# Kernel tuning notes

Measured on AMD Instinct MI355X. Metric: run time of the kernel, lower is better.

## Reference

```python
import jax, jax.numpy as jnp
import numpy as np

R, K = 16, 64  # rel_size (heads), key_size (head dim)
LN_EPS = 1e-5


def apply_rope(x, pos):
    # pos: [B,S,1,K], halves are sin/cos; x: [B,S,R,K]
    sin, cos = jnp.split(pos, 2, axis=-1)
    x0, x1 = jnp.split(x, 2, axis=-1)
    return jnp.concatenate([x0 * cos - x1 * sin, x0 * sin + x1 * cos], axis=-1)


def setup_inputs() -> dict:
    key = jax.random.key(0)
    ks = jax.random.split(key, 6)
    B, S, H = 2, 2048, 1024
    x = jax.random.normal(ks[0], (B, S, H), dtype=jnp.float32)
    pos = jax.random.uniform(ks[1], (B, S, 1, K), dtype=jnp.float32)
    W_qkv = jax.random.normal(ks[2], (H, R * K * 3), dtype=jnp.float32) * (H ** -0.5)
    b_qkv = jax.random.normal(ks[3], (R * K * 3,), dtype=jnp.float32) * 0.02
    W_out = jax.random.normal(ks[4], (R * K, H), dtype=jnp.float32) * ((R * K) ** -0.5)
    b_out = jax.random.normal(ks[5], (H,), dtype=jnp.float32) * 0.02
    ln_g = jnp.ones((H,), dtype=jnp.float32)
    ln_b = jnp.zeros((H,), dtype=jnp.float32)
    return {"x": x, "pos": pos, "W_qkv": W_qkv, "b_qkv": b_qkv,
            "W_out": W_out, "b_out": b_out, "ln_g": ln_g, "ln_b": ln_b}


def reference(x, pos, W_qkv, b_qkv, W_out, b_out, ln_g, ln_b):
    B, S, H = x.shape
    qkv = (x @ W_qkv + b_qkv).reshape(B, S, R, 3 * K)
    q, k, v = jnp.split(qkv, 3, axis=-1)  # each [B,S,R,K]
    k = k / jnp.linalg.norm(k, axis=-1, keepdims=True)
    q = apply_rope(q, pos)
    k = apply_rope(k, pos)
    # SDPA with scale=1 (as in the original call)
    scores = jnp.einsum('bqhd,bkhd->bhqk', q, k)
    attn = jax.nn.softmax(scores, axis=-1)
    ctx = jnp.einsum('bhqk,bkhd->bqhd', attn, v).reshape(B, S, R * K)
    postx = ctx @ W_out + b_out
    y = x + postx
    mu = jnp.mean(y, axis=-1, keepdims=True)
    var = jnp.mean(jnp.square(y - mu), axis=-1, keepdims=True)
    return (y - mu) * jax.lax.rsqrt(var + LN_EPS) * ln_g + ln_b
```

## Files before the change

kernel.cpp:

```cpp
#include <hip/hip_runtime.h>


#define B_   2
#define S_   2048
#define H_   1024
#define R_   16
#define BS_  (B_*S_)
#define NQKV 3072
#define LOG2E 1.44269504088896f

typedef float    floatx4 __attribute__((ext_vector_type(4)));
typedef _Float16 half8   __attribute__((ext_vector_type(8)));
typedef _Float16 half4   __attribute__((ext_vector_type(4)));
typedef __fp16   fp16x2  __attribute__((ext_vector_type(2)));

#if __has_builtin(__builtin_amdgcn_exp2f)
#define EXP2(x) __builtin_amdgcn_exp2f(x)
#else
#define EXP2(x) exp2f(x)
#endif

__device__ __forceinline__ void gl_lds16(const _Float16* g, _Float16* l) {
    __builtin_amdgcn_global_load_lds(
        (const __attribute__((address_space(1))) unsigned int*)g,
        (__attribute__((address_space(3))) unsigned int*)l, 16, 0, 0);
}

__global__ __launch_bounds__(256) void cast_f16_kernel(
    const float* __restrict__ in, _Float16* __restrict__ out, int n)
{
    int i = (blockIdx.x * 256 + threadIdx.x) * 4;
    if (i >= n) return;
    float4 v = *(const float4*)(in + i);
    half4 h;
    h.x = (_Float16)v.x; h.y = (_Float16)v.y; h.z = (_Float16)v.z; h.w = (_Float16)v.w;
    *(half4*)(out + i) = h;
}

__global__ __launch_bounds__(256) void transpose_cast_f16(
    const float* __restrict__ in, _Float16* __restrict__ out, int rows, int cols)
{
    __shared__ float tile[32][33];
    int bx = blockIdx.x * 32;
    int by = blockIdx.y * 32;
    int tx = threadIdx.x & 31, ty = threadIdx.x >> 5;
#pragma unroll
    for (int i = 0; i < 32; i += 8)
        tile[ty + i][tx] = in[(size_t)(by + ty + i) * cols + bx + tx];
    __syncthreads();
#pragma unroll
    for (int i = 0; i < 32; i += 8)
        out[(size_t)(bx + ty + i) * rows + by + tx] = (_Float16)tile[tx][ty + i];
}

__global__ __launch_bounds__(256) void gemm_f16_mfma(
    const _Float16* __restrict__ A, const _Float16* __restrict__ Bt,
    const float* __restrict__ bias, const float* __restrict__ resid,
    float* __restrict__ C, int M, int N, int Kd)
{
    __shared__ _Float16 Als[128 * 32];
    __shared__ _Float16 Bls[128 * 32];
    int tid  = threadIdx.x;
    int lane = tid & 63, w = tid >> 6;
    int wr = w >> 1, wc = w & 1;
    int fr = lane & 15, fq = lane >> 4;
    int m0 = blockIdx.y * 128, n0 = blockIdx.x * 128;

    floatx4 acc[4][4] = {};

    const _Float16* ga[2]; const _Float16* gb[2];
    _Float16 *la[2], *lb[2];
#pragma unroll
    for (int i2 = 0; i2 < 2; ++i2) {
        int ch = 2 * w + i2;
        int row = ch * 16 + (lane >> 2), col = (lane & 3) * 8;
        ga[i2] = A  + (size_t)(m0 + row) * Kd + col;
        gb[i2] = Bt + (size_t)(n0 + row) * Kd + col;
        la[i2] = Als + ch * 512;
        lb[i2] = Bls + ch * 512;
    }

    for (int k0 = 0; k0 < Kd; k0 += 32) {
        __syncthreads();
#pragma unroll
        for (int i2 = 0; i2 < 2; ++i2) {
            gl_lds16(ga[i2] + k0, la[i2]);
            gl_lds16(gb[i2] + k0, lb[i2]);
        }
        __syncthreads();
        half8 af[4], bf[4];
#pragma unroll
        for (int i = 0; i < 4; ++i)
            af[i] = *(const half8*)(Als + (wr * 64 + i * 16 + fr) * 32 + fq * 8);
#pragma unroll
        for (int j = 0; j < 4; ++j)
            bf[j] = *(const half8*)(Bls + (wc * 64 + j * 16 + fr) * 32 + fq * 8);
#pragma unroll
        for (int i = 0; i < 4; ++i)
#pragma unroll
            for (int j = 0; j < 4; ++j)
                acc[i][j] = __builtin_amdgcn_mfma_f32_16x16x32_f16(
                    af[i], bf[j], acc[i][j], 0, 0, 0);
    }

#pragma unroll
    for (int i = 0; i < 4; ++i)
#pragma unroll
        for (int j = 0; j < 4; ++j)
#pragma unroll
            for (int r2 = 0; r2 < 4; ++r2) {
                int row = m0 + wr * 64 + i * 16 + fq * 4 + r2;
                int col = n0 + wc * 64 + j * 16 + fr;
                float v = acc[i][j][r2] + bias[col];
                if (resid) v += resid[(size_t)row * N + col];
                C[(size_t)row * N + col] = v;
            }
}

__global__ __launch_bounds__(256) void rope_kernel(
    const float* __restrict__ qkv, const float* __restrict__ pos,
    _Float16* __restrict__ qt, _Float16* __restrict__ kt)
{
    int task = blockIdx.x * 4 + (threadIdx.x >> 6);
    int lane = threadIdx.x & 63;
    int r = task & 15, bs = task >> 4;
    int b = bs >> 11, s = bs & 2047;

    const float* base = qkv + (size_t)bs * NQKV + r * 192;
    float qv = base[lane];
    float kv = base[64 + lane];

    float ss = kv * kv;
#pragma unroll
    for (int off = 32; off > 0; off >>= 1) ss += __shfl_xor(ss, off);
    kv *= rsqrtf(ss);

    int j = lane & 31;
    float sn = pos[(size_t)bs * 64 + j];
    float cs = pos[(size_t)bs * 64 + 32 + j];
    float qp = __shfl_xor(qv, 32);
    float kp = __shfl_xor(kv, 32);
    float qo, ko;
    if (lane < 32) { qo = qv * cs - qp * sn; ko = kv * cs - kp * sn; }
    else           { qo = qp * sn + qv * cs; ko = kp * sn + kv * cs; }

    size_t oidx = ((size_t)(b * 16 + r) * S_ + s) * 64 + lane;
    qt[oidx] = (_Float16)(qo * LOG2E);
    kt[oidx] = (_Float16)ko;
}

__global__ __launch_bounds__(256) void vtrans_kernel(
    const float* __restrict__ qkv, _Float16* __restrict__ vt2)
{
    __shared__ float tile[64][65];
    int head = blockIdx.x, tau = blockIdx.y;
    int s0 = tau * 64;
    int b = head >> 4, rh = head & 15;
    int tx = threadIdx.x & 63, ty = threadIdx.x >> 6;
#pragma unroll
    for (int si = ty; si < 64; si += 4)
        tile[si][tx] = qkv[(size_t)(b * S_ + s0 + si) * NQKV + rh * 192 + 128 + tx];
    __syncthreads();
    int P = tx;
    int op = P >> 3;
    int hi = (P >> 2) & 1, lo = P & 3;
#pragma unroll
    for (int d = ty; d < 64; d += 4) {
        int ol = op ^ (d & 7);
        int key = 32 * (ol >> 2) + 16 * hi + 4 * (ol & 3) + lo;
        vt2[(((size_t)head * 32 + tau) * 64 + d) * 64 + P] = (_Float16)tile[key][d];
    }
}

__global__ __launch_bounds__(256) void attn_mfma_kernel(
    const _Float16* __restrict__ qt, const _Float16* __restrict__ kt,
    const _Float16* __restrict__ vt2, _Float16* __restrict__ ctx)
{
    __shared__ _Float16 Kls[64 * 64];
    __shared__ _Float16 Vls[64 * 64];

    int head = blockIdx.x, q0 = blockIdx.y * 128;
    int b = head >> 4, rh = head & 15;
    int tid = threadIdx.x, lane = tid & 63, w = tid >> 6;
    int g = lane >> 4, c = lane & 15;

    half8 qf[2][2];
    float mL[2], l_s[2] = {0.f, 0.f};
#pragma unroll
    for (int qg = 0; qg < 2; ++qg) {
        const _Float16* qp =
            qt + ((size_t)head * S_ + q0 + w * 32 + qg * 16 + c) * 64 + 8 * g;
        qf[qg][0] = *(const half8*)qp;
        qf[qg][1] = *(const half8*)(qp + 32);
        float qq = 0.f;
#pragma unroll
        for (int i = 0; i < 8; ++i) {
            float a = (float)qf[qg][0][i], b2 = (float)qf[qg][1][i];
            qq += a * a + b2 * b2;
        }
        qq += __shfl_xor(qq, 16);
        qq += __shfl_xor(qq, 32);
        mL[qg] = sqrtf(qq);
    }

    floatx4 o_acc[2][4] = {};

    const _Float16* kg[2]; const _Float16* vg[2];
    _Float16 *kl_[2], *vl_[2];
#pragma unroll
    for (int i2 = 0; i2 < 2; ++i2) {
        int ch = 2 * w + i2;
        int krow = ch * 8 + (lane >> 3);
        int koct = (lane & 7) ^ (lane >> 3);
        kg[i2] = kt + ((size_t)head * S_ + krow) * 64 + koct * 8;
        kl_[i2] = Kls + ch * 512;
        vg[i2] = vt2 + ((size_t)head * 32) * 4096 + ch * 512 + lane * 8;
        vl_[i2] = Vls + ch * 512;
    }

    int co = c & 7;

    for (int j0 = 0; j0 < S_; j0 += 64) {
        __syncthreads();
#pragma unroll
        for (int i2 = 0; i2 < 2; ++i2) {
            gl_lds16(kg[i2] + (size_t)j0 * 64, kl_[i2]);
            gl_lds16(vg[i2] + (size_t)(j0 >> 6) * 4096, vl_[i2]);
        }
        __syncthreads();

        half8 kfr[8];
#pragma unroll
        for (int t = 0; t < 4; ++t) {
            const _Float16* krow = Kls + (16 * t + c) * 64;
            kfr[2 * t]     = *(const half8*)(krow + ((g) ^ co) * 8);
            kfr[2 * t + 1] = *(const half8*)(krow + ((4 + g) ^ co) * 8);
        }

        union { half8 v; fp16x2 h2[4]; } pf[2][2];
#pragma unroll
        for (int qg = 0; qg < 2; ++qg) {
            floatx4 sacc[4];
#pragma unroll
            for (int t = 0; t < 4; ++t) {
                floatx4 z = {};
                z = __builtin_amdgcn_mfma_f32_16x16x32_f16(
                    kfr[2 * t], qf[qg][0], z, 0, 0, 0);
                z = __builtin_amdgcn_mfma_f32_16x16x32_f16(
                    kfr[2 * t + 1], qf[qg][1], z, 0, 0, 0);
                sacc[t] = z;
            }
            float mLq = mL[qg], ps = 0.f;
#pragma unroll
            for (int t = 0; t < 4; ++t)
#pragma unroll
                for (int r = 0; r < 4; ++r) {
                    float p = EXP2(sacc[t][r] - mLq);
                    sacc[t][r] = p;
                    ps += p;
                }
            l_s[qg] += ps;
            pf[qg][0].h2[0] = __builtin_amdgcn_cvt_pkrtz(sacc[0][0], sacc[0][1]);
            pf[qg][0].h2[1] = __builtin_amdgcn_cvt_pkrtz(sacc[0][2], sacc[0][3]);
            pf[qg][0].h2[2] = __builtin_amdgcn_cvt_pkrtz(sacc[1][0], sacc[1][1]);
            pf[qg][0].h2[3] = __builtin_amdgcn_cvt_pkrtz(sacc[1][2], sacc[1][3]);
            pf[qg][1].h2[0] = __builtin_amdgcn_cvt_pkrtz(sacc[2][0], sacc[2][1]);
            pf[qg][1].h2[1] = __builtin_amdgcn_cvt_pkrtz(sacc[2][2], sacc[2][3]);
            pf[qg][1].h2[2] = __builtin_amdgcn_cvt_pkrtz(sacc[3][0], sacc[3][1]);
            pf[qg][1].h2[3] = __builtin_amdgcn_cvt_pkrtz(sacc[3][2], sacc[3][3]);
        }

#pragma unroll
        for (int t = 0; t < 4; ++t) {
            const _Float16* vrow = Vls + (16 * t + c) * 64;
            half8 v0 = *(const half8*)(vrow + ((g) ^ co) * 8);
            half8 v1 = *(const half8*)(vrow + ((4 + g) ^ co) * 8);
#pragma unroll
            for (int qg = 0; qg < 2; ++qg) {
                o_acc[qg][t] = __builtin_amdgcn_mfma_f32_16x16x32_f16(
                    v0, pf[qg][0].v, o_acc[qg][t], 0, 0, 0);
                o_acc[qg][t] = __builtin_amdgcn_mfma_f32_16x16x32_f16(
                    v1, pf[qg][1].v, o_acc[qg][t], 0, 0, 0);
            }
        }
    }

#pragma unroll
    for (int qg = 0; qg < 2; ++qg) {
        float lt = l_s[qg];
        lt += __shfl_xor(lt, 16);
        lt += __shfl_xor(lt, 32);
        float inv = 1.f / lt;
        size_t rowbase =
            ((size_t)(b * S_ + q0 + w * 32 + qg * 16 + c)) * 1024 + rh * 64;
#pragma unroll
        for (int t = 0; t < 4; ++t) {
            union { half4 v; fp16x2 h2[2]; } e;
            e.h2[0] = __builtin_amdgcn_cvt_pkrtz(o_acc[qg][t][0] * inv,
                                                 o_acc[qg][t][1] * inv);
            e.h2[1] = __builtin_amdgcn_cvt_pkrtz(o_acc[qg][t][2] * inv,
                                                 o_acc[qg][t][3] * inv);
            *(half4*)(ctx + rowbase + 16 * t + 4 * g) = e.v;
        }
    }
}

__global__ __launch_bounds__(256) void ln_kernel(
    float* __restrict__ y, const float* __restrict__ g, const float* __restrict__ bb)
{
    int row = blockIdx.x, tid = threadIdx.x;
    float* p = y + (size_t)row * 1024;
    float4 v = ((const float4*)p)[tid];
    float sum = v.x + v.y + v.z + v.w;
    float sq  = v.x*v.x + v.y*v.y + v.z*v.z + v.w*v.w;
#pragma unroll
    for (int off = 32; off > 0; off >>= 1) {
        sum += __shfl_xor(sum, off);
        sq  += __shfl_xor(sq,  off);
    }
    __shared__ float rs[4], rq[4];
    int w = tid >> 6;
    if ((tid & 63) == 0) { rs[w] = sum; rq[w] = sq; }
    __syncthreads();
    sum = rs[0] + rs[1] + rs[2] + rs[3];
    sq  = rq[0] + rq[1] + rq[2] + rq[3];
    float mean = sum * (1.f / 1024.f);
    float var  = sq * (1.f / 1024.f) - mean * mean;
    float inv  = rsqrtf(var + 1e-5f);
    float4 gv = ((const float4*)g)[tid];
    float4 bv = ((const float4*)bb)[tid];
    v.x = (v.x - mean) * inv * gv.x + bv.x;
    v.y = (v.y - mean) * inv * gv.y + bv.y;
    v.z = (v.z - mean) * inv * gv.z + bv.z;
    v.w = (v.w - mean) * inv * gv.w + bv.w;
    ((float4*)p)[tid] = v;
}

extern "C" void kernel_launch(void* const* d_in, const int* in_sizes, int n_in,
                              void* d_out, int out_size, void* d_ws, size_t ws_size,
                              hipStream_t stream)
{
    const float* x     = (const float*)d_in[0];
    const float* pos   = (const float*)d_in[1];
    const float* W_qkv = (const float*)d_in[2];
    const float* b_qkv = (const float*)d_in[3];
    const float* W_out = (const float*)d_in[4];
    const float* b_out = (const float*)d_in[5];
    const float* ln_g  = (const float*)d_in[6];
    const float* ln_b  = (const float*)d_in[7];
    float* out = (float*)d_out;

    char* ws = (char*)d_ws;
    _Float16* x_h    = (_Float16*)(ws);
    _Float16* wqkv_t = (_Float16*)(ws + ((size_t)8  << 20));
    _Float16* wout_t = (_Float16*)(ws + ((size_t)14 << 20));
    float*    qkv    = (float*)   (ws + ((size_t)16 << 20));
    _Float16* qt_h   = (_Float16*)(ws + ((size_t)64 << 20));
    _Float16* kt_h   = (_Float16*)(ws + ((size_t)72 << 20));
    _Float16* vt2_h  = (_Float16*)(ws + ((size_t)80 << 20));
    _Float16* ctx_h  = (_Float16*)(ws + ((size_t)88 << 20));

    cast_f16_kernel<<<4096, 256, 0, stream>>>(x, x_h, BS_ * H_);
    transpose_cast_f16<<<dim3(96, 32), 256, 0, stream>>>(W_qkv, wqkv_t, H_, NQKV);
    transpose_cast_f16<<<dim3(32, 32), 256, 0, stream>>>(W_out, wout_t, H_, H_);

    gemm_f16_mfma<<<dim3(NQKV / 128, BS_ / 128), 256, 0, stream>>>(
        x_h, wqkv_t, b_qkv, nullptr, qkv, BS_, NQKV, H_);

    rope_kernel<<<BS_ * R_ / 4, 256, 0, stream>>>(qkv, pos, qt_h, kt_h);
    vtrans_kernel<<<dim3(32, 32), 256, 0, stream>>>(qkv, vt2_h);

    attn_mfma_kernel<<<dim3(32, 16), 256, 0, stream>>>(qt_h, kt_h, vt2_h, ctx_h);

    gemm_f16_mfma<<<dim3(H_ / 128, BS_ / 128), 256, 0, stream>>>(
        ctx_h, wout_t, b_out, x, out, BS_, H_, H_);

    ln_kernel<<<BS_, 256, 0, stream>>>(out, ln_g, ln_b);
}
```

Measured before the change: 236.7 us.

## Double-buffer attention K/V tiles, fuse RoPE with V transpose, split-K output GEMM

The attention kernel now keeps two LDS buffers for K and V. It prefetches the next tile while computing the current one, which leaves one barrier per iteration instead of two. The RoPE/normalize kernel and the V transpose kernel are merged into one prep kernel. The output projection GEMM is split into two K halves written to separate partial buffers; these reuse the qkv workspace, which is dead by then. The LayerNorm kernel sums the halves before normalizing. This doubles the grid for the small output GEMM, at the cost of writing and reading an extra partial buffer.

```diff
diff --git a/kernel.cpp b/kernel.cpp
--- a/kernel.cpp
+++ b/kernel.cpp
@@ -56,7 +56,7 @@
 __global__ __launch_bounds__(256) void gemm_f16_mfma(
     const _Float16* __restrict__ A, const _Float16* __restrict__ Bt,
     const float* __restrict__ bias, const float* __restrict__ resid,
-    float* __restrict__ C, int M, int N, int Kd)
+    float* __restrict__ C, int M, int N, int Kd, int kPerSplit)
 {
     __shared__ _Float16 Als[128 * 32];
     __shared__ _Float16 Bls[128 * 32];
@@ -65,6 +65,9 @@
     int wr = w >> 1, wc = w & 1;
     int fr = lane & 15, fq = lane >> 4;
     int m0 = blockIdx.y * 128, n0 = blockIdx.x * 128;
+    int z  = blockIdx.z;
+    int kBeg = z * kPerSplit, kEnd = kBeg + kPerSplit;
+    float* Cz = C + (size_t)z * M * N;
 
     floatx4 acc[4][4] = {};
 
@@ -80,7 +83,7 @@
         lb[i2] = Bls + ch * 512;
     }
 
-    for (int k0 = 0; k0 < Kd; k0 += 32) {
+    for (int k0 = kBeg; k0 < kEnd; k0 += 32) {
         __syncthreads();
 #pragma unroll
         for (int i2 = 0; i2 < 2; ++i2) {
@@ -111,64 +114,66 @@
             for (int r2 = 0; r2 < 4; ++r2) {
                 int row = m0 + wr * 64 + i * 16 + fq * 4 + r2;
                 int col = n0 + wc * 64 + j * 16 + fr;
-                float v = acc[i][j][r2] + bias[col];
-                if (resid) v += resid[(size_t)row * N + col];
-                C[(size_t)row * N + col] = v;
+                float v = acc[i][j][r2];
+                if (z == 0) {
+                    v += bias[col];
+                    if (resid) v += resid[(size_t)row * N + col];
+                }
+                Cz[(size_t)row * N + col] = v;
             }
 }
 
-__global__ __launch_bounds__(256) void rope_kernel(
+__global__ __launch_bounds__(256) void prep_kernel(
     const float* __restrict__ qkv, const float* __restrict__ pos,
-    _Float16* __restrict__ qt, _Float16* __restrict__ kt)
-{
-    int task = blockIdx.x * 4 + (threadIdx.x >> 6);
-    int lane = threadIdx.x & 63;
-    int r = task & 15, bs = task >> 4;
-    int b = bs >> 11, s = bs & 2047;
-
-    const float* base = qkv + (size_t)bs * NQKV + r * 192;
-    float qv = base[lane];
-    float kv = base[64 + lane];
-
-    float ss = kv * kv;
-#pragma unroll
-    for (int off = 32; off > 0; off >>= 1) ss += __shfl_xor(ss, off);
-    kv *= rsqrtf(ss);
-
-    int j = lane & 31;
-    float sn = pos[(size_t)bs * 64 + j];
-    float cs = pos[(size_t)bs * 64 + 32 + j];
-    float qp = __shfl_xor(qv, 32);
-    float kp = __shfl_xor(kv, 32);
-    float qo, ko;
-    if (lane < 32) { qo = qv * cs - qp * sn; ko = kv * cs - kp * sn; }
-    else           { qo = qp * sn + qv * cs; ko = kp * sn + kv * cs; }
-
-    size_t oidx = ((size_t)(b * 16 + r) * S_ + s) * 64 + lane;
-    qt[oidx] = (_Float16)(qo * LOG2E);
-    kt[oidx] = (_Float16)ko;
-}
-
-__global__ __launch_bounds__(256) void vtrans_kernel(
-    const float* __restrict__ qkv, _Float16* __restrict__ vt2)
+    _Float16* __restrict__ qt, _Float16* __restrict__ kt,
+    _Float16* __restrict__ vt2)
 {
     __shared__ float tile[64][65];
     int head = blockIdx.x, tau = blockIdx.y;
     int s0 = tau * 64;
     int b = head >> 4, rh = head & 15;
-    int tx = threadIdx.x & 63, ty = threadIdx.x >> 6;
-#pragma unroll
-    for (int si = ty; si < 64; si += 4)
-        tile[si][tx] = qkv[(size_t)(b * S_ + s0 + si) * NQKV + rh * 192 + 128 + tx];
+    int lane = threadIdx.x & 63, w = threadIdx.x >> 6;
+
+#pragma unroll
+    for (int si = w; si < 64; si += 4)
+        tile[si][lane] = qkv[(size_t)(b * S_ + s0 + si) * NQKV + rh * 192 + 128 + lane];
     __syncthreads();
-    int P = tx;
-    int op = P >> 3;
-    int hi = (P >> 2) & 1, lo = P & 3;
-#pragma unroll
-    for (int d = ty; d < 64; d += 4) {
-        int ol = op ^ (d & 7);
-        int key = 32 * (ol >> 2) + 16 * hi + 4 * (ol & 3) + lo;
-        vt2[(((size_t)head * 32 + tau) * 64 + d) * 64 + P] = (_Float16)tile[key][d];
+    {
+        int P = lane;
+        int op = P >> 3;
+        int hi = (P >> 2) & 1, lo = P & 3;
+#pragma unroll
+        for (int d = w; d < 64; d += 4) {
+            int ol = op ^ (d & 7);
+            int key = 32 * (ol >> 2) + 16 * hi + 4 * (ol & 3) + lo;
+            vt2[(((size_t)head * 32 + tau) * 64 + d) * 64 + P] = (_Float16)tile[key][d];
+        }
+    }
+
+    for (int i = 0; i < 16; ++i) {
+        int s = s0 + w * 16 + i;
+        int bs = b * S_ + s;
+        const float* base = qkv + (size_t)bs * NQKV + rh * 192;
+        float qv = base[lane];
+        float kv = base[64 + lane];
+
+        float ss = kv * kv;
+#pragma unroll
+        for (int off = 32; off > 0; off >>= 1) ss += __shfl_xor(ss, off);
+        kv *= rsqrtf(ss);
+
+        int j = lane & 31;
+        float sn = pos[(size_t)bs * 64 + j];
+        float cs = pos[(size_t)bs * 64 + 32 + j];
+        float qp = __shfl_xor(qv, 32);
+        float kp = __shfl_xor(kv, 32);
+        float qo, ko;
+        if (lane < 32) { qo = qv * cs - qp * sn; ko = kv * cs - kp * sn; }
+        else           { qo = qp * sn + qv * cs; ko = kp * sn + kv * cs; }
+
+        size_t oidx = ((size_t)head * S_ + s) * 64 + lane;
+        qt[oidx] = (_Float16)(qo * LOG2E);
+        kt[oidx] = (_Float16)ko;
     }
 }
 
@@ -176,8 +181,8 @@
     const _Float16* __restrict__ qt, const _Float16* __restrict__ kt,
     const _Float16* __restrict__ vt2, _Float16* __restrict__ ctx)
 {
-    __shared__ _Float16 Kls[64 * 64];
-    __shared__ _Float16 Vls[64 * 64];
+    __shared__ _Float16 Kls[2][4096];
+    __shared__ _Float16 Vls[2][4096];
 
     int head = blockIdx.x, q0 = blockIdx.y * 128;
     int b = head >> 4, rh = head & 15;
@@ -206,33 +211,42 @@
     floatx4 o_acc[2][4] = {};
 
     const _Float16* kg[2]; const _Float16* vg[2];
-    _Float16 *kl_[2], *vl_[2];
+    int loff[2];
 #pragma unroll
     for (int i2 = 0; i2 < 2; ++i2) {
         int ch = 2 * w + i2;
         int krow = ch * 8 + (lane >> 3);
         int koct = (lane & 7) ^ (lane >> 3);
         kg[i2] = kt + ((size_t)head * S_ + krow) * 64 + koct * 8;
-        kl_[i2] = Kls + ch * 512;
         vg[i2] = vt2 + ((size_t)head * 32) * 4096 + ch * 512 + lane * 8;
-        vl_[i2] = Vls + ch * 512;
+        loff[i2] = ch * 512;
     }
 
     int co = c & 7;
 
-    for (int j0 = 0; j0 < S_; j0 += 64) {
+#pragma unroll
+    for (int i2 = 0; i2 < 2; ++i2) {
+        gl_lds16(kg[i2], &Kls[0][loff[i2]]);
+        gl_lds16(vg[i2], &Vls[0][loff[i2]]);
+    }
+
+    for (int jt = 0; jt < 32; ++jt) {
+        int cur = jt & 1;
         __syncthreads();
-#pragma unroll
-        for (int i2 = 0; i2 < 2; ++i2) {
-            gl_lds16(kg[i2] + (size_t)j0 * 64, kl_[i2]);
-            gl_lds16(vg[i2] + (size_t)(j0 >> 6) * 4096, vl_[i2]);
-        }
-        __syncthreads();
+        if (jt + 1 < 32) {
+#pragma unroll
+            for (int i2 = 0; i2 < 2; ++i2) {
+                gl_lds16(kg[i2] + (size_t)(jt + 1) * 4096, &Kls[cur ^ 1][loff[i2]]);
+                gl_lds16(vg[i2] + (size_t)(jt + 1) * 4096, &Vls[cur ^ 1][loff[i2]]);
+            }
+        }
+        const _Float16* Kbuf = Kls[cur];
+        const _Float16* Vbuf = Vls[cur];
 
         half8 kfr[8];
 #pragma unroll
         for (int t = 0; t < 4; ++t) {
-            const _Float16* krow = Kls + (16 * t + c) * 64;
+            const _Float16* krow = Kbuf + (16 * t + c) * 64;
             kfr[2 * t]     = *(const half8*)(krow + ((g) ^ co) * 8);
             kfr[2 * t + 1] = *(const half8*)(krow + ((4 + g) ^ co) * 8);
         }
@@ -272,7 +286,7 @@
 
 #pragma unroll
         for (int t = 0; t < 4; ++t) {
-            const _Float16* vrow = Vls + (16 * t + c) * 64;
+            const _Float16* vrow = Vbuf + (16 * t + c) * 64;
             half8 v0 = *(const half8*)(vrow + ((g) ^ co) * 8);
             half8 v1 = *(const half8*)(vrow + ((4 + g) ^ co) * 8);
 #pragma unroll
@@ -305,12 +319,16 @@
     }
 }
 
-__global__ __launch_bounds__(256) void ln_kernel(
-    float* __restrict__ y, const float* __restrict__ g, const float* __restrict__ bb)
+__global__ __launch_bounds__(256) void ln2_kernel(
+    const float* __restrict__ y0, const float* __restrict__ y1,
+    const float* __restrict__ g, const float* __restrict__ bb,
+    float* __restrict__ out)
 {
     int row = blockIdx.x, tid = threadIdx.x;
-    float* p = y + (size_t)row * 1024;
-    float4 v = ((const float4*)p)[tid];
+    float4 a = ((const float4*)(y0 + (size_t)row * 1024))[tid];
+    float4 b4 = ((const float4*)(y1 + (size_t)row * 1024))[tid];
+    float4 v;
+    v.x = a.x + b4.x; v.y = a.y + b4.y; v.z = a.z + b4.z; v.w = a.w + b4.w;
     float sum = v.x + v.y + v.z + v.w;
     float sq  = v.x*v.x + v.y*v.y + v.z*v.z + v.w*v.w;
 #pragma unroll
@@ -333,7 +351,7 @@
     v.y = (v.y - mean) * inv * gv.y + bv.y;
     v.z = (v.z - mean) * inv * gv.z + bv.z;
     v.w = (v.w - mean) * inv * gv.w + bv.w;
-    ((float4*)p)[tid] = v;
+    ((float4*)(out + (size_t)row * 1024))[tid] = v;
 }
 
 extern "C" void kernel_launch(void* const* d_in, const int* in_sizes, int n_in,
@@ -355,6 +373,7 @@
     _Float16* wqkv_t = (_Float16*)(ws + ((size_t)8  << 20));
     _Float16* wout_t = (_Float16*)(ws + ((size_t)14 << 20));
     float*    qkv    = (float*)   (ws + ((size_t)16 << 20));
+    float*    ypart  = (float*)   (ws + ((size_t)16 << 20));
     _Float16* qt_h   = (_Float16*)(ws + ((size_t)64 << 20));
     _Float16* kt_h   = (_Float16*)(ws + ((size_t)72 << 20));
     _Float16* vt2_h  = (_Float16*)(ws + ((size_t)80 << 20));
@@ -364,16 +383,16 @@
     transpose_cast_f16<<<dim3(96, 32), 256, 0, stream>>>(W_qkv, wqkv_t, H_, NQKV);
     transpose_cast_f16<<<dim3(32, 32), 256, 0, stream>>>(W_out, wout_t, H_, H_);
 
-    gemm_f16_mfma<<<dim3(NQKV / 128, BS_ / 128), 256, 0, stream>>>(
-        x_h, wqkv_t, b_qkv, nullptr, qkv, BS_, NQKV, H_);
-
-    rope_kernel<<<BS_ * R_ / 4, 256, 0, stream>>>(qkv, pos, qt_h, kt_h);
-    vtrans_kernel<<<dim3(32, 32), 256, 0, stream>>>(qkv, vt2_h);
+    gemm_f16_mfma<<<dim3(NQKV / 128, BS_ / 128, 1), 256, 0, stream>>>(
+        x_h, wqkv_t, b_qkv, nullptr, qkv, BS_, NQKV, H_, H_);
+
+    prep_kernel<<<dim3(32, 32), 256, 0, stream>>>(qkv, pos, qt_h, kt_h, vt2_h);
 
     attn_mfma_kernel<<<dim3(32, 16), 256, 0, stream>>>(qt_h, kt_h, vt2_h, ctx_h);
 
-    gemm_f16_mfma<<<dim3(H_ / 128, BS_ / 128), 256, 0, stream>>>(
-        ctx_h, wout_t, b_out, x, out, BS_, H_, H_);
-
-    ln_kernel<<<BS_, 256, 0, stream>>>(out, ln_g, ln_b);
-}
+    gemm_f16_mfma<<<dim3(H_ / 128, BS_ / 128, 2), 256, 0, stream>>>(
+        ctx_h, wout_t, b_out, x, ypart, BS_, H_, H_, H_ / 2);
+
+    ln2_kernel<<<BS_, 256, 0, stream>>>(
+        ypart, ypart + (size_t)BS_ * H_, ln_g, ln_b, out);
+}
```

New measurement: 258.4 us. 1.09x slower.

## Double-buffer GEMM LDS tiles and store QKV projection as fp16

Applied to the files above, without the earlier changes.

The GEMM kernel now uses two LDS buffers per operand. It prefetches the next K-slice with global_load_lds while MFMAs run on the current slice, and it drops one barrier per iteration. The QKV GEMM writes its output as fp16 instead of fp32, and the rope and V-transpose kernels read that fp16 buffer. This halves intermediate memory traffic. The cost is double the GEMM LDS footprint and a small extra rounding of q/k/v before the key normalisation.

```diff
diff --git a/kernel.cpp b/kernel.cpp
--- a/kernel.cpp
+++ b/kernel.cpp
@@ -53,13 +53,14 @@
         out[(size_t)(bx + ty + i) * rows + by + tx] = (_Float16)tile[tx][ty + i];
 }
 
+template <bool F16OUT>
 __global__ __launch_bounds__(256) void gemm_f16_mfma(
     const _Float16* __restrict__ A, const _Float16* __restrict__ Bt,
     const float* __restrict__ bias, const float* __restrict__ resid,
-    float* __restrict__ C, int M, int N, int Kd)
-{
-    __shared__ _Float16 Als[128 * 32];
-    __shared__ _Float16 Bls[128 * 32];
+    float* __restrict__ Cf, _Float16* __restrict__ Ch, int M, int N, int Kd)
+{
+    __shared__ _Float16 Als[2][4096];
+    __shared__ _Float16 Bls[2][4096];
     int tid  = threadIdx.x;
     int lane = tid & 63, w = tid >> 6;
     int wr = w >> 1, wc = w & 1;
@@ -69,32 +70,43 @@
     floatx4 acc[4][4] = {};
 
     const _Float16* ga[2]; const _Float16* gb[2];
-    _Float16 *la[2], *lb[2];
+    int loff[2];
 #pragma unroll
     for (int i2 = 0; i2 < 2; ++i2) {
         int ch = 2 * w + i2;
         int row = ch * 16 + (lane >> 2), col = (lane & 3) * 8;
         ga[i2] = A  + (size_t)(m0 + row) * Kd + col;
         gb[i2] = Bt + (size_t)(n0 + row) * Kd + col;
-        la[i2] = Als + ch * 512;
-        lb[i2] = Bls + ch * 512;
-    }
-
-    for (int k0 = 0; k0 < Kd; k0 += 32) {
+        loff[i2] = ch * 512;
+    }
+
+    int nIter = Kd >> 5;
+#pragma unroll
+    for (int i2 = 0; i2 < 2; ++i2) {
+        gl_lds16(ga[i2], &Als[0][loff[i2]]);
+        gl_lds16(gb[i2], &Bls[0][loff[i2]]);
+    }
+
+    for (int it = 0; it < nIter; ++it) {
+        int cur = it & 1;
         __syncthreads();
-#pragma unroll
-        for (int i2 = 0; i2 < 2; ++i2) {
-            gl_lds16(ga[i2] + k0, la[i2]);
-            gl_lds16(gb[i2] + k0, lb[i2]);
-        }
-        __syncthreads();
+        if (it + 1 < nIter) {
+            int k1 = (it + 1) << 5;
+#pragma unroll
+            for (int i2 = 0; i2 < 2; ++i2) {
+                gl_lds16(ga[i2] + k1, &Als[cur ^ 1][loff[i2]]);
+                gl_lds16(gb[i2] + k1, &Bls[cur ^ 1][loff[i2]]);
+            }
+        }
+        const _Float16* Ab = Als[cur];
+        const _Float16* Bb = Bls[cur];
         half8 af[4], bf[4];
 #pragma unroll
         for (int i = 0; i < 4; ++i)
-            af[i] = *(const half8*)(Als + (wr * 64 + i * 16 + fr) * 32 + fq * 8);
+            af[i] = *(const half8*)(Ab + (wr * 64 + i * 16 + fr) * 32 + fq * 8);
 #pragma unroll
         for (int j = 0; j < 4; ++j)
-            bf[j] = *(const half8*)(Bls + (wc * 64 + j * 16 + fr) * 32 + fq * 8);
+            bf[j] = *(const half8*)(Bb + (wc * 64 + j * 16 + fr) * 32 + fq * 8);
 #pragma unroll
         for (int i = 0; i < 4; ++i)
 #pragma unroll
@@ -112,13 +124,17 @@
                 int row = m0 + wr * 64 + i * 16 + fq * 4 + r2;
                 int col = n0 + wc * 64 + j * 16 + fr;
                 float v = acc[i][j][r2] + bias[col];
-                if (resid) v += resid[(size_t)row * N + col];
-                C[(size_t)row * N + col] = v;
+                if constexpr (F16OUT) {
+                    Ch[(size_t)row * N + col] = (_Float16)v;
+                } else {
+                    if (resid) v += resid[(size_t)row * N + col];
+                    Cf[(size_t)row * N + col] = v;
+                }
             }
 }
 
 __global__ __launch_bounds__(256) void rope_kernel(
-    const float* __restrict__ qkv, const float* __restrict__ pos,
+    const _Float16* __restrict__ qkvh, const float* __restrict__ pos,
     _Float16* __restrict__ qt, _Float16* __restrict__ kt)
 {
     int task = blockIdx.x * 4 + (threadIdx.x >> 6);
@@ -126,9 +142,9 @@
     int r = task & 15, bs = task >> 4;
     int b = bs >> 11, s = bs & 2047;
 
-    const float* base = qkv + (size_t)bs * NQKV + r * 192;
-    float qv = base[lane];
-    float kv = base[64 + lane];
+    const _Float16* base = qkvh + (size_t)bs * NQKV + r * 192;
+    float qv = (float)base[lane];
+    float kv = (float)base[64 + lane];
 
     float ss = kv * kv;
 #pragma unroll
@@ -150,7 +166,7 @@
 }
 
 __global__ __launch_bounds__(256) void vtrans_kernel(
-    const float* __restrict__ qkv, _Float16* __restrict__ vt2)
+    const _Float16* __restrict__ qkvh, _Float16* __restrict__ vt2)
 {
     __shared__ float tile[64][65];
     int head = blockIdx.x, tau = blockIdx.y;
@@ -159,7 +175,7 @@
     int tx = threadIdx.x & 63, ty = threadIdx.x >> 6;
 #pragma unroll
     for (int si = ty; si < 64; si += 4)
-        tile[si][tx] = qkv[(size_t)(b * S_ + s0 + si) * NQKV + rh * 192 + 128 + tx];
+        tile[si][tx] = (float)qkvh[(size_t)(b * S_ + s0 + si) * NQKV + rh * 192 + 128 + tx];
     __syncthreads();
     int P = tx;
     int op = P >> 3;
@@ -354,26 +370,26 @@
     _Float16* x_h    = (_Float16*)(ws);
     _Float16* wqkv_t = (_Float16*)(ws + ((size_t)8  << 20));
     _Float16* wout_t = (_Float16*)(ws + ((size_t)14 << 20));
-    float*    qkv    = (float*)   (ws + ((size_t)16 << 20));
-    _Float16* qt_h   = (_Float16*)(ws + ((size_t)64 << 20));
-    _Float16* kt_h   = (_Float16*)(ws + ((size_t)72 << 20));
-    _Float16* vt2_h  = (_Float16*)(ws + ((size_t)80 << 20));
-    _Float16* ctx_h  = (_Float16*)(ws + ((size_t)88 << 20));
+    _Float16* qkvh   = (_Float16*)(ws + ((size_t)16 << 20));
+    _Float16* qt_h   = (_Float16*)(ws + ((size_t)40 << 20));
+    _Float16* kt_h   = (_Float16*)(ws + ((size_t)48 << 20));
+    _Float16* vt2_h  = (_Float16*)(ws + ((size_t)56 << 20));
+    _Float16* ctx_h  = (_Float16*)(ws + ((size_t)64 << 20));
 
     cast_f16_kernel<<<4096, 256, 0, stream>>>(x, x_h, BS_ * H_);
     transpose_cast_f16<<<dim3(96, 32), 256, 0, stream>>>(W_qkv, wqkv_t, H_, NQKV);
     transpose_cast_f16<<<dim3(32, 32), 256, 0, stream>>>(W_out, wout_t, H_, H_);
 
-    gemm_f16_mfma<<<dim3(NQKV / 128, BS_ / 128), 256, 0, stream>>>(
-        x_h, wqkv_t, b_qkv, nullptr, qkv, BS_, NQKV, H_);
-
-    rope_kernel<<<BS_ * R_ / 4, 256, 0, stream>>>(qkv, pos, qt_h, kt_h);
-    vtrans_kernel<<<dim3(32, 32), 256, 0, stream>>>(qkv, vt2_h);
+    gemm_f16_mfma<true><<<dim3(NQKV / 128, BS_ / 128), 256, 0, stream>>>(
+        x_h, wqkv_t, b_qkv, nullptr, nullptr, qkvh, BS_, NQKV, H_);
+
+    rope_kernel<<<BS_ * R_ / 4, 256, 0, stream>>>(qkvh, pos, qt_h, kt_h);
+    vtrans_kernel<<<dim3(32, 32), 256, 0, stream>>>(qkvh, vt2_h);
 
     attn_mfma_kernel<<<dim3(32, 16), 256, 0, stream>>>(qt_h, kt_h, vt2_h, ctx_h);
 
-    gemm_f16_mfma<<<dim3(H_ / 128, BS_ / 128), 256, 0, stream>>>(
-        ctx_h, wout_t, b_out, x, out, BS_, H_, H_);
+    gemm_f16_mfma<false><<<dim3(H_ / 128, BS_ / 128), 256, 0, stream>>>(
+        ctx_h, wout_t, b_out, x, out, nullptr, BS_, H_, H_);
 
     ln_kernel<<<BS_, 256, 0, stream>>>(out, ln_g, ln_b);
 }
```

Result: no change. 232.4 us (-1.8%).
